# Kernel tuning notes

Hardware: AMD Instinct MI355X
Metric: run time of the kernel (lower is better)

The kernel has to match this reference:

```python
import jax, jax.numpy as jnp
import numpy as np

FP16_MAX = 65504.0


def setup_inputs() -> dict:
    key = jax.random.key(0)
    k1, k2, k3 = jax.random.split(key, 3)
    N, B, M = 1024, 128, 256
    # anchors: (N, 2) positive widths/heights
    anchors = jax.random.uniform(k1, (N, 2), dtype=jnp.float32, minval=0.05, maxval=1.0)
    # gt_boxes: (B, M, 4) valid corner-format boxes (xmin, ymin, xmax, ymax)
    xy = jax.random.uniform(k2, (B, M, 2), dtype=jnp.float32, minval=0.0, maxval=1.0)
    wh = jax.random.uniform(k3, (B, M, 2), dtype=jnp.float32, minval=0.05, maxval=1.0)
    gt_boxes = jnp.concatenate([xy, xy + wh], axis=-1)
    return {"anchors": anchors, "gt_boxes": gt_boxes}


def reference(anchors, gt_boxes):
    # corner -> (w, h) of gt boxes (only w,h are used by the Matcher)
    xmin, ymin, xmax, ymax = jnp.split(gt_boxes, 4, axis=-1)  # each (B, M, 1)
    gtw = (xmax - xmin)[..., 0]  # (B, M)
    gth = (ymax - ymin)[..., 0]  # (B, M)
    # shift gt boxes to be centered at origin: corners of (w, h)
    bl, bt, br, bb = -0.5 * gtw, -0.5 * gth, 0.5 * gtw, 0.5 * gth  # (B, M)

    # anchors (N, 2) -> zero-centered corner boxes
    aw = anchors[:, 0]  # (N,)
    ah = anchors[:, 1]  # (N,)
    al, at, ar, ab = -0.5 * aw, -0.5 * ah, 0.5 * aw, 0.5 * ah  # (N,)

    # broadcasted pairwise intersection: (B, N, M)
    left = jnp.maximum(al[None, :, None], bl[:, None, :])
    right = jnp.minimum(ar[None, :, None], br[:, None, :])
    top = jnp.maximum(at[None, :, None], bt[:, None, :])
    bot = jnp.minimum(ab[None, :, None], bb[:, None, :])
    iw = jnp.clip(right - left, 0.0, FP16_MAX)
    ih = jnp.clip(bot - top, 0.0, FP16_MAX)
    inter = iw * ih  # (B, N, M)

    area_a = (aw * ah)[None, :, None]   # (1, N, 1)
    area_b = (gtw * gth)[:, None, :]    # (B, 1, M)
    union = area_a + area_b - inter
    ious = inter / union  # (B, N, M)

    matches = jnp.argmax(ious, axis=1)  # (B, M), best anchor per gt box
    return matches, ious
```

## Files before the change

kernel.cpp:

```cpp
#include <hip/hip_runtime.h>


#define N_ANCH 1024
#define B_SZ   128
#define M_SZ   256
#define NWAVES 8
#define NPW    (N_ANCH / NWAVES)

__global__ __launch_bounds__(512) void matcher_kernel(
    const float* __restrict__ anchors,
    const float* __restrict__ gt,
    float* __restrict__ out)
{
    __shared__ float2 s_anch[N_ANCH];
    __shared__ float  s_val[NWAVES * 128];
    __shared__ int    s_idx[NWAVES * 128];

    const int tid  = threadIdx.x;
    const int lane = tid & 63;
    const int w    = tid >> 6;
    const int b    = blockIdx.x >> 1;
    const int half = blockIdx.x & 1;

    const float2* a2 = (const float2*)anchors;
    for (int i = tid; i < N_ANCH; i += 512) s_anch[i] = a2[i];

    const int m0 = half * 128 + lane * 2;
    const float4* g4 = (const float4*)gt;
    float4 g0 = g4[b * M_SZ + m0];
    float4 g1 = g4[b * M_SZ + m0 + 1];
    const float gtw0 = g0.z - g0.x, gth0 = g0.w - g0.y;
    const float gtw1 = g1.z - g1.x, gth1 = g1.w - g1.y;
    const float areab0 = gtw0 * gth0, areab1 = gtw1 * gth1;

    __syncthreads();

    float bv0 = -1.0f, bv1 = -1.0f;
    int   bi0 = 0,     bi1 = 0;
    float* __restrict__ ious = out + (size_t)B_SZ * M_SZ;
    const int n_begin = w * NPW;
    float* __restrict__ row = ious + (size_t)(b * N_ANCH + n_begin) * M_SZ + m0;

    #pragma unroll 4
    for (int n = n_begin; n < n_begin + NPW; ++n) {
        float2 a = s_anch[n];
        float areaa = a.x * a.y;

        float iw0 = fminf(a.x, gtw0), ih0 = fminf(a.y, gth0);
        float inter0 = iw0 * ih0;
        float iou0 = __fdividef(inter0, areaa + areab0 - inter0);

        float iw1 = fminf(a.x, gtw1), ih1 = fminf(a.y, gth1);
        float inter1 = iw1 * ih1;
        float iou1 = __fdividef(inter1, areaa + areab1 - inter1);

        if (iou0 > bv0) { bv0 = iou0; bi0 = n; }
        if (iou1 > bv1) { bv1 = iou1; bi1 = n; }

        *(float2*)row = make_float2(iou0, iou1);
        row += M_SZ;
    }

    s_val[w * 128 + lane * 2]     = bv0;
    s_idx[w * 128 + lane * 2]     = bi0;
    s_val[w * 128 + lane * 2 + 1] = bv1;
    s_idx[w * 128 + lane * 2 + 1] = bi1;
    __syncthreads();

    if (tid < 128) {
        float bv = s_val[tid];
        int   bi = s_idx[tid];
        for (int ww = 1; ww < NWAVES; ++ww) {
            float v = s_val[ww * 128 + tid];
            int   ix = s_idx[ww * 128 + tid];
            if (v > bv) { bv = v; bi = ix; }
        }
        out[b * M_SZ + half * 128 + tid] = (float)bi;
    }
}

extern "C" void kernel_launch(void* const* d_in, const int* in_sizes, int n_in,
                              void* d_out, int out_size, void* d_ws, size_t ws_size,
                              hipStream_t stream) {
    const float* anchors = (const float*)d_in[0];
    const float* gt      = (const float*)d_in[1];
    float* out = (float*)d_out;

    dim3 grid(B_SZ * 2);
    dim3 block(512);
    matcher_kernel<<<grid, block, 0, stream>>>(anchors, gt, out);
}
```

Measured before the change: 139.9 us.

## Split anchor range across blocks with two-kernel argmax reduction and float4 stores

Each block now covers one batch, all 256 gt boxes and a quarter of the anchors, rather than half the gt boxes and all anchors. Each thread computes four IoUs per anchor and writes them with one float4 store. Per-block partial argmax results go to workspace, and a second kernel reduces them across the four anchor quarters. This doubles the grid to spread the store-bound IoU writes over more CUs and widens each store, at the cost of an extra kernel launch and workspace traffic.

```diff
diff --git a/kernel.cpp b/kernel.cpp
--- a/kernel.cpp
+++ b/kernel.cpp
@@ -4,79 +4,113 @@
 #define N_ANCH 1024
 #define B_SZ   128
 #define M_SZ   256
+#define NQ     4
+#define NPB    (N_ANCH / NQ)
 #define NWAVES 8
-#define NPW    (N_ANCH / NWAVES)
+#define NPW    (NPB / NWAVES)
 
-__global__ __launch_bounds__(512) void matcher_kernel(
+__global__ __launch_bounds__(512) void iou_kernel(
     const float* __restrict__ anchors,
     const float* __restrict__ gt,
-    float* __restrict__ out)
+    float* __restrict__ out,
+    float* __restrict__ ws_val,
+    int*   __restrict__ ws_idx)
 {
-    __shared__ float2 s_anch[N_ANCH];
-    __shared__ float  s_val[NWAVES * 128];
-    __shared__ int    s_idx[NWAVES * 128];
+    __shared__ float2 s_anch[NPB];
+    __shared__ float  s_val[NWAVES * M_SZ];
+    __shared__ int    s_idx[NWAVES * M_SZ];
 
     const int tid  = threadIdx.x;
     const int lane = tid & 63;
     const int w    = tid >> 6;
-    const int b    = blockIdx.x >> 1;
-    const int half = blockIdx.x & 1;
+    const int b    = blockIdx.x >> 2;
+    const int q    = blockIdx.x & 3;
 
-    const float2* a2 = (const float2*)anchors;
-    for (int i = tid; i < N_ANCH; i += 512) s_anch[i] = a2[i];
+    if (tid < NPB) s_anch[tid] = ((const float2*)anchors)[q * NPB + tid];
 
-    const int m0 = half * 128 + lane * 2;
-    const float4* g4 = (const float4*)gt;
-    float4 g0 = g4[b * M_SZ + m0];
-    float4 g1 = g4[b * M_SZ + m0 + 1];
-    const float gtw0 = g0.z - g0.x, gth0 = g0.w - g0.y;
-    const float gtw1 = g1.z - g1.x, gth1 = g1.w - g1.y;
-    const float areab0 = gtw0 * gth0, areab1 = gtw1 * gth1;
+    const int m0 = lane * 4;
+    const float4* g4 = (const float4*)gt + b * M_SZ + m0;
+    float gtw[4], gth[4], areab[4];
+    #pragma unroll
+    for (int j = 0; j < 4; ++j) {
+        float4 g = g4[j];
+        gtw[j]   = g.z - g.x;
+        gth[j]   = g.w - g.y;
+        areab[j] = gtw[j] * gth[j];
+    }
 
     __syncthreads();
 
-    float bv0 = -1.0f, bv1 = -1.0f;
-    int   bi0 = 0,     bi1 = 0;
-    float* __restrict__ ious = out + (size_t)B_SZ * M_SZ;
-    const int n_begin = w * NPW;
-    float* __restrict__ row = ious + (size_t)(b * N_ANCH + n_begin) * M_SZ + m0;
+    float bv[4] = {-1.f, -1.f, -1.f, -1.f};
+    int   bi[4] = {0, 0, 0, 0};
+
+    const int n_begin = q * NPB + w * NPW;
+    float* __restrict__ row = out + (size_t)B_SZ * M_SZ
+                            + (size_t)(b * N_ANCH + n_begin) * M_SZ + m0;
+    const int a_base = w * NPW;
+
+    #define IOU1(J, DST)                                                    \
+    {                                                                       \
+        float iw    = fminf(a.x, gtw[J]);                                   \
+        float ih    = fminf(a.y, gth[J]);                                   \
+        float inter = iw * ih;                                              \
+        float iou   = __fdividef(inter, areaa + areab[J] - inter);          \
+        DST = iou;                                                          \
+        if (iou > bv[J]) { bv[J] = iou; bi[J] = n; }   \
+    }
 
     #pragma unroll 4
-    for (int n = n_begin; n < n_begin + NPW; ++n) {
-        float2 a = s_anch[n];
+    for (int i = 0; i < NPW; ++i) {
+        const int n = n_begin + i;
+        float2 a = s_anch[a_base + i];
         float areaa = a.x * a.y;
-
-        float iw0 = fminf(a.x, gtw0), ih0 = fminf(a.y, gth0);
-        float inter0 = iw0 * ih0;
-        float iou0 = __fdividef(inter0, areaa + areab0 - inter0);
-
-        float iw1 = fminf(a.x, gtw1), ih1 = fminf(a.y, gth1);
-        float inter1 = iw1 * ih1;
-        float iou1 = __fdividef(inter1, areaa + areab1 - inter1);
-
-        if (iou0 > bv0) { bv0 = iou0; bi0 = n; }
-        if (iou1 > bv1) { bv1 = iou1; bi1 = n; }
-
-        *(float2*)row = make_float2(iou0, iou1);
+        float4 r;
+        IOU1(0, r.x)
+        IOU1(1, r.y)
+        IOU1(2, r.z)
+        IOU1(3, r.w)
+        *(float4*)row = r;
         row += M_SZ;
     }
+    #undef IOU1
 
-    s_val[w * 128 + lane * 2]     = bv0;
-    s_idx[w * 128 + lane * 2]     = bi0;
-    s_val[w * 128 + lane * 2 + 1] = bv1;
-    s_idx[w * 128 + lane * 2 + 1] = bi1;
+    #pragma unroll
+    for (int j = 0; j < 4; ++j) {
+        s_val[w * M_SZ + m0 + j] = bv[j];
+        s_idx[w * M_SZ + m0 + j] = bi[j];
+    }
     __syncthreads();
 
-    if (tid < 128) {
-        float bv = s_val[tid];
-        int   bi = s_idx[tid];
+    if (tid < M_SZ) {
+        float v  = s_val[tid];
+        int   ix = s_idx[tid];
+        #pragma unroll
         for (int ww = 1; ww < NWAVES; ++ww) {
-            float v = s_val[ww * 128 + tid];
-            int   ix = s_idx[ww * 128 + tid];
-            if (v > bv) { bv = v; bi = ix; }
+            float v2 = s_val[ww * M_SZ + tid];
+            if (v2 > v) { v = v2; ix = s_idx[ww * M_SZ + tid]; }
         }
-        out[b * M_SZ + half * 128 + tid] = (float)bi;
+        ws_val[(b * NQ + q) * M_SZ + tid] = v;
+        ws_idx[(b * NQ + q) * M_SZ + tid] = ix;
     }
+}
+
+__global__ __launch_bounds__(512) void match_kernel(
+    const float* __restrict__ ws_val,
+    const int*   __restrict__ ws_idx,
+    float* __restrict__ out)
+{
+    const int t = blockIdx.x * 512 + threadIdx.x;
+    const int b = t >> 8;
+    const int m = t & (M_SZ - 1);
+    const int base = b * NQ * M_SZ + m;
+    float v  = ws_val[base];
+    int   ix = ws_idx[base];
+    #pragma unroll
+    for (int q = 1; q < NQ; ++q) {
+        float v2 = ws_val[base + q * M_SZ];
+        if (v2 > v) { v = v2; ix = ws_idx[base + q * M_SZ]; }
+    }
+    out[t] = (float)ix;
 }
 
 extern "C" void kernel_launch(void* const* d_in, const int* in_sizes, int n_in,
@@ -86,7 +120,12 @@
     const float* gt      = (const float*)d_in[1];
     float* out = (float*)d_out;
 
-    dim3 grid(B_SZ * 2);
-    dim3 block(512);
-    matcher_kernel<<<grid, block, 0, stream>>>(anchors, gt, out);
+    float* ws_val = (float*)d_ws;
+    int*   ws_idx = (int*)((char*)d_ws
+                   + (size_t)B_SZ * NQ * M_SZ * sizeof(float));
+
+    iou_kernel<<<dim3(B_SZ * NQ), dim3(512), 0, stream>>>(
+        anchors, gt, out, ws_val, ws_idx);
+    match_kernel<<<dim3(B_SZ * M_SZ / 512), dim3(512), 0, stream>>>(
+        ws_val, ws_idx, out);
 }
```

New measurement: 138.3 us (median of 2 runs). Within noise of the previous version (-1.2%).
